# Kernel tuning notes

Measured on AMD Instinct MI355X. Metric: run time of the kernel, lower is better.

The kernel has to match this reference:

```python
import jax, jax.numpy as jnp
import numpy as np

N_NODES = 50000
N_EDGES = 800000
N_GRAPHS = 16
F_IN = 128
E_DIM = 16
HID = 32
HEADS = 2
EPS_BN = 1e-5


def gatv2_conv(x, edge_index, edge_attr, Wl, bl, Wr, br, We, att, bias, heads, out_ch):
    """PyG GATv2Conv (share_weights=False, concat=True, add_self_loops=True, fill_value='mean')."""
    n = x.shape[0]
    src, dst = edge_index[0], edge_index[1]
    loop = jnp.arange(n)
    src = jnp.concatenate([src, loop])
    dst = jnp.concatenate([dst, loop])
    ea = jnp.concatenate([edge_attr, jnp.broadcast_to(edge_attr.mean(0), (n, edge_attr.shape[1]))])
    x_l = (x @ Wl + bl).reshape(n, heads, out_ch)   # source transform
    x_r = (x @ Wr + br).reshape(n, heads, out_ch)   # target transform
    e = (ea @ We).reshape(-1, heads, out_ch)
    m = jax.nn.leaky_relu(x_l[src] + x_r[dst] + e, 0.2)      # [E, H, C]
    alpha = (m * att[None]).sum(-1)                          # [E, H]
    amax = jax.ops.segment_max(alpha, dst, num_segments=n)
    ex = jnp.exp(alpha - amax[dst])
    denom = jax.ops.segment_sum(ex, dst, num_segments=n)
    alpha = ex / (denom[dst] + 1e-16)
    out = jax.ops.segment_sum(x_l[src] * alpha[..., None], dst, num_segments=n)
    return out.reshape(n, heads * out_ch) + bias


def batch_norm(x, g, b):
    mu = x.mean(0)
    var = jnp.var(x, axis=0)  # biased, as torch BatchNorm1d training mode
    return (x - mu) * jax.lax.rsqrt(var + EPS_BN) * g + b


def setup_inputs() -> dict:
    key = jax.random.key(0)
    ks = jax.random.split(key, 24)
    s = 0.1
    d1 = HID * HEADS  # 64
    inp = {
        'x': jax.random.normal(ks[0], (N_NODES, F_IN), jnp.float32),
        'edge_index': jax.random.randint(ks[1], (2, N_EDGES), 0, N_NODES),
        'edge_attr': jax.random.normal(ks[2], (N_EDGES, E_DIM), jnp.float32),
        'batch': jnp.sort(jax.random.randint(ks[3], (N_NODES,), 0, N_GRAPHS)),
        'skip1_W': jax.random.normal(ks[4], (F_IN, d1)) * s,
        'skip1_b': jnp.zeros((d1,)),
        'conv1_Wl': jax.random.normal(ks[5], (F_IN, d1)) * s,
        'conv1_bl': jnp.zeros((d1,)),
        'conv1_Wr': jax.random.normal(ks[6], (F_IN, d1)) * s,
        'conv1_br': jnp.zeros((d1,)),
        'conv1_We': jax.random.normal(ks[7], (E_DIM, d1)) * s,
        'conv1_att': jax.random.normal(ks[8], (HEADS, HID)) * s,
        'conv1_bias': jnp.zeros((d1,)),
        'bn1_g': jnp.ones((d1,)),
        'bn1_b': jnp.zeros((d1,)),
        'skip2_W': jax.random.normal(ks[9], (d1, HID)) * s,
        'skip2_b': jnp.zeros((HID,)),
        'conv2_Wl': jax.random.normal(ks[10], (d1, HID)) * s,
        'conv2_bl': jnp.zeros((HID,)),
        'conv2_Wr': jax.random.normal(ks[11], (d1, HID)) * s,
        'conv2_br': jnp.zeros((HID,)),
        'conv2_We': jax.random.normal(ks[12], (E_DIM, HID)) * s,
        'conv2_att': jax.random.normal(ks[13], (1, HID)) * s,
        'conv2_bias': jnp.zeros((HID,)),
        'bn2_g': jnp.ones((HID,)),
        'bn2_b': jnp.zeros((HID,)),
    }
    return inp


def reference(x, edge_index, edge_attr, batch,
              skip1_W, skip1_b, conv1_Wl, conv1_bl, conv1_Wr, conv1_br, conv1_We, conv1_att, conv1_bias, bn1_g, bn1_b,
              skip2_W, skip2_b, conv2_Wl, conv2_bl, conv2_Wr, conv2_br, conv2_We, conv2_att, conv2_bias, bn2_g, bn2_b):
    h_proj = x @ skip1_W + skip1_b
    h = gatv2_conv(x, edge_index, edge_attr, conv1_Wl, conv1_bl, conv1_Wr, conv1_br, conv1_We, conv1_att, conv1_bias, HEADS, HID)
    h = jax.nn.elu(batch_norm(h, bn1_g, bn1_b) + h_proj)
    h_proj = h @ skip2_W + skip2_b
    h2 = gatv2_conv(h, edge_index, edge_attr, conv2_Wl, conv2_bl, conv2_Wr, conv2_br, conv2_We, conv2_att, conv2_bias, 1, HID)
    h2 = jax.nn.elu(batch_norm(h2, bn2_g, bn2_b) + h_proj)
    ones = jnp.ones((h2.shape[0],), h2.dtype)
    counts = jax.ops.segment_sum(ones, batch, num_segments=N_GRAPHS)
    x_mean = jax.ops.segment_sum(h2, batch, num_segments=N_GRAPHS) / jnp.maximum(counts, 1.0)[:, None]
    x_max = jax.ops.segment_max(h2, batch, num_segments=N_GRAPHS)
    x_max = jnp.where(counts[:, None] > 0, x_max, 0.0)
    return jnp.concatenate([x_mean, x_max], axis=1)
```

## Files before the change

### kernel.cpp

```cpp
#include <hip/hip_runtime.h>
#include <hip/hip_bf16.h>

#define NE 800000
#define NN 50000
#define NG 16
#define ETOT (NE + NN)

typedef unsigned short u16;
typedef __attribute__((ext_vector_type(8))) short short8;
typedef __attribute__((ext_vector_type(4))) float float4v;

__device__ __forceinline__ float b2f(u16 u) {
  return __uint_as_float(((unsigned)u) << 16);
}
__device__ __forceinline__ u16 f2b(float f) {
  __hip_bfloat16 b = __float2bfloat16(f);
  return *(u16*)&b;
}
__device__ __forceinline__ void cv8(uint4 v, float* o) {
  o[0] = __uint_as_float(v.x << 16);
  o[1] = __uint_as_float(v.x & 0xFFFF0000u);
  o[2] = __uint_as_float(v.y << 16);
  o[3] = __uint_as_float(v.y & 0xFFFF0000u);
  o[4] = __uint_as_float(v.z << 16);
  o[5] = __uint_as_float(v.z & 0xFFFF0000u);
  o[6] = __uint_as_float(v.w << 16);
  o[7] = __uint_as_float(v.w & 0xFFFF0000u);
}
__device__ __forceinline__ unsigned pk2(float a, float b) {
  return (unsigned)f2b(a) | ((unsigned)f2b(b) << 16);
}
__device__ __forceinline__ unsigned f2key(float f) {
  unsigned u = __float_as_uint(f);
  return (u & 0x80000000u) ? ~u : (u | 0x80000000u);
}
__device__ __forceinline__ float key2f(unsigned k) {
  unsigned u = (k & 0x80000000u) ? (k ^ 0x80000000u) : ~k;
  return __uint_as_float(u);
}
__device__ __forceinline__ int plaus(unsigned h) {
  unsigned eh = (h >> 7) & 0xFF;
  return (h == 0) || (eh >= 100 && eh <= 140);
}
__device__ __forceinline__ float lrelu(float v) {
  return (v > 0.f) ? v : 0.2f * v;
}

#define NDEG 8
#define NPOOL 16
#define LOG2E 1.4426950408889634f

__global__ __launch_bounds__(256) void k_init(uint4* __restrict__ zbase, int zcnt16,
                                              const unsigned* __restrict__ a,
                                              const unsigned* __restrict__ b,
                                              const unsigned* __restrict__ c,
                                              int* __restrict__ flags) {
  uint4 z = {0, 0, 0, 0};
  for (int i = blockIdx.x * 256 + threadIdx.x; i < zcnt16; i += gridDim.x * 256)
    zbase[i] = z;
  if (blockIdx.x != 0) return;
  __shared__ int cnt[3];
  if (threadIdx.x < 3) cnt[threadIdx.x] = 0;
  __syncthreads();
  const unsigned* arr[3] = {a, b, c};
  for (int k = 0; k < 3; k++) {
    int ok = 0;
    for (int i = threadIdx.x; i < 4096; i += 256) {
      unsigned w = arr[k][i];
      ok += (plaus(w & 0xFFFFu) && plaus(w >> 16)) ? 1 : 0;
    }
    atomicAdd(&cnt[k], ok);
  }
  __syncthreads();
  if (threadIdx.x == 0) {
    int f0 = cnt[0] > 2048, f1 = cnt[1] > 2048, f2 = cnt[2] > 2048;
    flags[0] = f0;
    flags[1] = f1;
    flags[2] = f2;
    flags[3] = f0 && f1 && f2;
  }
}

__global__ __launch_bounds__(256) void k_hist(const int* __restrict__ ei,
                                              int* __restrict__ deg8) {
  int gt = blockIdx.x * 256 + threadIdx.x;
  if (gt >= ETOT) return;
  int dst = (gt < NE) ? ei[NE + gt] : gt - NE;
  atomicAdd(&deg8[(blockIdx.x & (NDEG - 1)) * NN + dst], 1);
}

__global__ __launch_bounds__(256) void k_colsum_xsplit(
    const void* __restrict__ ea, const void* __restrict__ xin,
    const int* __restrict__ flg, float* __restrict__ mean_part,
    u16* __restrict__ xh, u16* __restrict__ xlo) {
  int gt = blockIdx.x * 256 + threadIdx.x;
  bool eb = flg[2] != 0;
  int col = gt & 15;
  int row = gt >> 4;
  int rstride = (gridDim.x * 256) >> 4;
  float s = 0.f;
  if (eb) {
    const u16* p = (const u16*)ea;
    for (int e = row; e < NE; e += rstride) s += b2f(p[(size_t)e * 16 + col]);
  } else {
    const float* p = (const float*)ea;
    for (int e = row; e < NE; e += rstride) s += p[(size_t)e * 16 + col];
  }
  __shared__ float ls[256];
  ls[threadIdx.x] = s;
  __syncthreads();
  if (threadIdx.x < 16) {
    float t = 0.f;
    for (int i = threadIdx.x; i < 256; i += 16) t += ls[i];
    atomicAdd(&mean_part[(blockIdx.x & 63) * 16 + threadIdx.x], t);
  }
  if (flg[0] == 0) {
    const float4* xp4 = (const float4*)xin;
    const int nch = NN * 32;
    int stride = gridDim.x * 256;
    for (int i = gt; i < nch; i += stride) {
      float4 v = xp4[i];
      u16 h0 = f2b(v.x), h1 = f2b(v.y), h2 = f2b(v.z), h3 = f2b(v.w);
      u16 l0 = f2b(v.x - b2f(h0));
      u16 l1 = f2b(v.y - b2f(h1));
      u16 l2 = f2b(v.z - b2f(h2));
      u16 l3 = f2b(v.w - b2f(h3));
      uint2 ho, lo2;
      ho.x = (unsigned)h0 | ((unsigned)h1 << 16);
      ho.y = (unsigned)h2 | ((unsigned)h3 << 16);
      lo2.x = (unsigned)l0 | ((unsigned)l1 << 16);
      lo2.y = (unsigned)l2 | ((unsigned)l3 << 16);
      *(uint2*)(xh + (size_t)i * 4) = ho;
      *(uint2*)(xlo + (size_t)i * 4) = lo2;
    }
  }
}

#define SCAN_NT ((NN + 1023) / 1024)

__global__ __launch_bounds__(256) void k_scansum(const int* __restrict__ deg8,
                                                 const float* __restrict__ mean_part,
                                                 float* __restrict__ mean_sums,
                                                 int* __restrict__ tile_tot) {
  int t = threadIdx.x;
  if (blockIdx.x == 0 && t < 16) {
    float s = 0.f;
#pragma unroll
    for (int j = 0; j < 64; j++) s += mean_part[j * 16 + t];
    mean_sums[t] = s;
  }
  int lane = t & 63;
  int wv = t >> 6;
  int idx = blockIdx.x * 1024 + t * 4;
  int s4 = 0;
  if (idx + 3 < NN) {
#pragma unroll
    for (int c = 0; c < NDEG; c++) {
      int4 dc = *(const int4*)(deg8 + c * NN + idx);
      s4 += dc.x + dc.y + dc.z + dc.w;
    }
  } else {
#pragma unroll
    for (int c = 0; c < NDEG; c++) {
      if (idx + 0 < NN) s4 += deg8[c * NN + idx + 0];
      if (idx + 1 < NN) s4 += deg8[c * NN + idx + 1];
      if (idx + 2 < NN) s4 += deg8[c * NN + idx + 2];
      if (idx + 3 < NN) s4 += deg8[c * NN + idx + 3];
    }
  }
  int r = s4;
#pragma unroll
  for (int ofs = 1; ofs < 64; ofs <<= 1) r += __shfl_xor(r, ofs, 64);
  __shared__ int wsum[4];
  if (lane == 0) wsum[wv] = r;
  __syncthreads();
  if (t == 0) tile_tot[blockIdx.x] = wsum[0] + wsum[1] + wsum[2] + wsum[3];
}

__global__ __launch_bounds__(256) void k_scanwrite(const int* __restrict__ deg8,
                                                   const int* __restrict__ tile_tot,
                                                   int* __restrict__ start,
                                                   int* __restrict__ cursor) {
  __shared__ int sbase;
  __shared__ int wsum[4];
  int t = threadIdx.x;
  int lane = t & 63;
  int wv = t >> 6;
  if (wv == 0) {
    int v = (lane < SCAN_NT) ? tile_tot[lane] : 0;
    int sc = v;
#pragma unroll
    for (int ofs = 1; ofs < 64; ofs <<= 1) {
      int u = __shfl_up(sc, ofs, 64);
      if (lane >= ofs) sc += u;
    }
    if (lane == (int)blockIdx.x) sbase = sc - v;
    if (blockIdx.x == 0 && lane == SCAN_NT - 1) start[NN] = sc;
  }
  int idx = blockIdx.x * 1024 + t * 4;
  int4 d = {0, 0, 0, 0};
  if (idx + 3 < NN) {
#pragma unroll
    for (int c = 0; c < NDEG; c++) {
      int4 dc = *(const int4*)(deg8 + c * NN + idx);
      d.x += dc.x; d.y += dc.y; d.z += dc.z; d.w += dc.w;
    }
  } else {
#pragma unroll
    for (int c = 0; c < NDEG; c++) {
      if (idx + 0 < NN) d.x += deg8[c * NN + idx + 0];
      if (idx + 1 < NN) d.y += deg8[c * NN + idx + 1];
      if (idx + 2 < NN) d.z += deg8[c * NN + idx + 2];
      if (idx + 3 < NN) d.w += deg8[c * NN + idx + 3];
    }
  }
  int s4 = d.x + d.y + d.z + d.w;
  int sc = s4;
#pragma unroll
  for (int ofs = 1; ofs < 64; ofs <<= 1) {
    int v = __shfl_up(sc, ofs, 64);
    if (lane >= ofs) sc += v;
  }
  if (lane == 63) wsum[wv] = sc;
  __syncthreads();
  int wbase = 0;
#pragma unroll
  for (int w = 0; w < 4; w++)
    if (w < wv) wbase += wsum[w];
  int excl = sbase + wbase + (sc - s4);
  int4 st;
  st.x = excl;
  st.y = excl + d.x;
  st.z = st.y + d.y;
  st.w = st.z + d.z;
  if (idx + 3 < NN) {
    *(int4*)(start + idx) = st;
    *(int4*)(cursor + idx) = st;
  } else {
    if (idx + 0 < NN) { start[idx + 0] = st.x; cursor[idx + 0] = st.x; }
    if (idx + 1 < NN) { start[idx + 1] = st.y; cursor[idx + 1] = st.y; }
    if (idx + 2 < NN) { start[idx + 2] = st.z; cursor[idx + 2] = st.z; }
    if (idx + 3 < NN) { start[idx + 3] = st.w; cursor[idx + 3] = st.w; }
  }
}

template <int K, int N, int RPB>
__device__ __forceinline__ void gemm_direct(
    const void* __restrict__ W, const void* __restrict__ bb, bool wb,
    const u16* __restrict__ xh, const u16* __restrict__ xlo, bool has_lo,
    u16* __restrict__ out, int tile) {
  constexpr int CT = N / 16;
  constexpr int WPC = 4 / CT;
  constexpr int KK = K / 32;
  int lane = threadIdx.x & 63;
  int wave = threadIdx.x >> 6;
  int col = lane & 15;
  int quad = lane >> 4;
  int ct = wave % CT;
  int rt_off = wave / CT;
  short8 bh[KK], bl[KK];
#pragma unroll
  for (int kk = 0; kk < KK; kk++) {
    short8 th, tl;
#pragma unroll
    for (int j = 0; j < 8; j++) {
      int k = kk * 32 + quad * 8 + j;
      float w = wb ? b2f(((const u16*)W)[k * N + ct * 16 + col])
                   : ((const float*)W)[k * N + ct * 16 + col];
      u16 hb = f2b(w);
      th[j] = (short)hb;
      tl[j] = (short)f2b(w - b2f(hb));
    }
    bh[kk] = th;
    bl[kk] = tl;
  }
  float bias = wb ? b2f(((const u16*)bb)[ct * 16 + col])
                  : ((const float*)bb)[ct * 16 + col];
  int rt0 = tile * RPB;
  for (int i = rt_off; i < RPB; i += WPC) {
    int rt = rt0 + i;
    int row = rt * 16 + col;
    float4v acc = {0.f, 0.f, 0.f, 0.f};
#pragma unroll
    for (int kk = 0; kk < KK; kk++) {
      short8 afh = *(const short8*)(xh + (size_t)row * K + kk * 32 + quad * 8);
      acc = __builtin_amdgcn_mfma_f32_16x16x32_bf16(afh, bh[kk], acc, 0, 0, 0);
      if (has_lo) {
        short8 afl = *(const short8*)(xlo + (size_t)row * K + kk * 32 + quad * 8);
        acc = __builtin_amdgcn_mfma_f32_16x16x32_bf16(afl, bh[kk], acc, 0, 0, 0);
      }
      if (!wb)
        acc = __builtin_amdgcn_mfma_f32_16x16x32_bf16(afh, bl[kk], acc, 0, 0, 0);
    }
#pragma unroll
    for (int r = 0; r < 4; r++) {
      int orow = rt * 16 + quad * 4 + r;
      out[(size_t)orow * N + ct * 16 + col] = f2b(acc[r] + bias);
    }
  }
}

template <int K, int N, int TILES, int RPB>
__global__ __launch_bounds__(256) void k_lin1(
    const void* __restrict__ xin, const u16* __restrict__ xh,
    const u16* __restrict__ xlo, const int* __restrict__ flg,
    const void* W0, const void* W1, const void* W2,
    const void* b0, const void* b1, const void* b2,
    u16* __restrict__ o0, u16* __restrict__ o1, u16* __restrict__ o2) {
  int lidx = blockIdx.x;
  int wset = lidx / TILES;
  int tile = lidx % TILES;
  bool wb = flg[1] != 0;
  bool xb = flg[0] != 0;
  const void* W = wset == 0 ? W0 : (wset == 1 ? W1 : W2);
  const void* bb = wset == 0 ? b0 : (wset == 1 ? b1 : b2);
  u16* out = wset == 0 ? o0 : (wset == 1 ? o1 : o2);
  const u16* ah = xb ? (const u16*)xin : xh;
  gemm_direct<K, N, RPB>(W, bb, wb, ah, xlo, !xb, out, tile);
}

__global__ __launch_bounds__(256) void k_buildcsr_pay(
    const int* __restrict__ ei, const void* __restrict__ eattr,
    const int* __restrict__ flg, const float* __restrict__ mean_sums,
    int* __restrict__ cursor, int* __restrict__ csr_src,
    u16* __restrict__ ea16) {
  int e = blockIdx.x * 256 + threadIdx.x;
  if (e >= ETOT) return;
  bool eb = flg[2] != 0;
  int src, dst;
  if (e < NE) { src = ei[e]; dst = ei[NE + e]; } else { src = dst = e - NE; }
  float rec[16];
  if (e < NE) {
    if (eb) {
      const uint4* q = (const uint4*)((const u16*)eattr + (size_t)e * 16);
      cv8(q[0], rec);
      cv8(q[1], rec + 8);
    } else {
      const float* q = (const float*)eattr + (size_t)e * 16;
#pragma unroll
      for (int k = 0; k < 16; k++) rec[k] = q[k];
    }
  } else {
#pragma unroll
    for (int k = 0; k < 16; k++) rec[k] = mean_sums[k] * (1.0f / NE);
  }
  int pos = atomicAdd(&cursor[dst], 1);
  csr_src[pos] = src;
  u16 rb[16];
#pragma unroll
  for (int k = 0; k < 16; k++) rb[k] = f2b(rec[k]);
  uint4* dp = (uint4*)(ea16 + (size_t)pos * 16);
  dp[0] = *(uint4*)rb;
  dp[1] = *(uint4*)(rb + 8);
}

__global__ __launch_bounds__(256) void k_buildcsr(const int* __restrict__ ei,
                                                  int* __restrict__ cursor,
                                                  uint2* __restrict__ csr) {
  int e = blockIdx.x * 256 + threadIdx.x;
  if (e >= ETOT) return;
  int src, dst;
  if (e < NE) { src = ei[e]; dst = ei[NE + e]; } else { src = dst = e - NE; }
  int pos = atomicAdd(&cursor[dst], 1);
  uint2 r; r.x = (unsigned)src; r.y = (unsigned)e;
  csr[pos] = r;
}

__global__ __launch_bounds__(256) void k_ewgemm(
    const u16* __restrict__ ea, const int* __restrict__ flg,
    const void* We1, const void* We2,
    u16* __restrict__ ew1, u16* __restrict__ ew2) {
  bool wb = flg[1] != 0;
  int lane = threadIdx.x & 63;
  int col = lane & 15;
  int quad = lane >> 4;
  short8 b1h[4], b1l[4], b2h[2], b2l[2];
#pragma unroll
  for (int ct = 0; ct < 4; ct++) {
    short8 th, tl;
#pragma unroll
    for (int j = 0; j < 8; j++) {
      int k = quad * 8 + j;
      float w = 0.f;
      if (k < 16)
        w = wb ? b2f(((const u16*)We1)[k * 64 + ct * 16 + col])
               : ((const float*)We1)[k * 64 + ct * 16 + col];
      u16 hb = f2b(w);
      th[j] = (short)hb;
      tl[j] = (short)f2b(w - b2f(hb));
    }
    b1h[ct] = th; b1l[ct] = tl;
  }
#pragma unroll
  for (int ct = 0; ct < 2; ct++) {
    short8 th, tl;
#pragma unroll
    for (int j = 0; j < 8; j++) {
      int k = quad * 8 + j;
      float w = 0.f;
      if (k < 16)
        w = wb ? b2f(((const u16*)We2)[k * 32 + ct * 16 + col])
               : ((const float*)We2)[k * 32 + ct * 16 + col];
      u16 hb = f2b(w);
      th[j] = (short)hb;
      tl[j] = (short)f2b(w - b2f(hb));
    }
    b2h[ct] = th; b2l[ct] = tl;
  }
  int nw = (gridDim.x * 256) >> 6;
  int wid = (blockIdx.x * 256 + threadIdx.x) >> 6;
  const int NT = ETOT / 16;
  for (int rt = wid; rt < NT; rt += nw) {
    int row = rt * 16 + col;
    short8 af = {0, 0, 0, 0, 0, 0, 0, 0};
    if (quad < 2) af = *(const short8*)(ea + (size_t)row * 16 + quad * 8);
#pragma unroll
    for (int ct = 0; ct < 4; ct++) {
      float4v acc = {0.f, 0.f, 0.f, 0.f};
      acc = __builtin_amdgcn_mfma_f32_16x16x32_bf16(af, b1h[ct], acc, 0, 0, 0);
      acc = __builtin_amdgcn_mfma_f32_16x16x32_bf16(af, b1l[ct], acc, 0, 0, 0);
#pragma unroll
      for (int r = 0; r < 4; r++)
        ew1[(size_t)(rt * 16 + quad * 4 + r) * 64 + ct * 16 + col] = f2b(acc[r]);
    }
#pragma unroll
    for (int ct = 0; ct < 2; ct++) {
      float4v acc = {0.f, 0.f, 0.f, 0.f};
      acc = __builtin_amdgcn_mfma_f32_16x16x32_bf16(af, b2h[ct], acc, 0, 0, 0);
      acc = __builtin_amdgcn_mfma_f32_16x16x32_bf16(af, b2l[ct], acc, 0, 0, 0);
#pragma unroll
      for (int r = 0; r < 4; r++)
        ew2[(size_t)(rt * 16 + quad * 4 + r) * 32 + ct * 16 + col] = f2b(acc[r]);
    }
  }
}

template <int K, int N, int RPB>
__global__ __launch_bounds__(256) void k_lin3b(
    const void* __restrict__ xin, const int* __restrict__ flg,
    const void* W0, const void* W1, const void* W2,
    const void* b0, const void* b1, const void* b2,
    u16* __restrict__ o0, u16* __restrict__ o1, u16* __restrict__ o2, int M) {
  (void)M;
  bool wb = flg[1] != 0;
  const void* W = blockIdx.y == 0 ? W0 : (blockIdx.y == 1 ? W1 : W2);
  const void* bb = blockIdx.y == 0 ? b0 : (blockIdx.y == 1 ? b1 : b2);
  u16* out = blockIdx.y == 0 ? o0 : (blockIdx.y == 1 ? o1 : o2);
  gemm_direct<K, N, RPB>(W, bb, wb, (const u16*)xin, nullptr, false, out,
                         blockIdx.x);
}

__device__ __forceinline__ float dot16b(const u16* __restrict__ p,
                                        const float* __restrict__ W) {
  float ea[16];
  const uint4* q = (const uint4*)p;
  cv8(q[0], ea);
  cv8(q[1], ea + 8);
  float s = 0.f;
#pragma unroll
  for (int k = 0; k < 16; k++) s += ea[k] * W[k];
  return s;
}
__device__ __forceinline__ float dot16u(const u16* __restrict__ p,
                                        const float* __restrict__ W) {
  const uint4* q = (const uint4*)p;
  uint4 A = q[0], B = q[1];
  unsigned w0 = (unsigned)__builtin_amdgcn_readfirstlane((int)A.x);
  unsigned w1 = (unsigned)__builtin_amdgcn_readfirstlane((int)A.y);
  unsigned w2 = (unsigned)__builtin_amdgcn_readfirstlane((int)A.z);
  unsigned w3 = (unsigned)__builtin_amdgcn_readfirstlane((int)A.w);
  unsigned w4 = (unsigned)__builtin_amdgcn_readfirstlane((int)B.x);
  unsigned w5 = (unsigned)__builtin_amdgcn_readfirstlane((int)B.y);
  unsigned w6 = (unsigned)__builtin_amdgcn_readfirstlane((int)B.z);
  unsigned w7 = (unsigned)__builtin_amdgcn_readfirstlane((int)B.w);
  float s = 0.f;
  s += __uint_as_float(w0 << 16) * W[0];
  s += __uint_as_float(w0 & 0xFFFF0000u) * W[1];
  s += __uint_as_float(w1 << 16) * W[2];
  s += __uint_as_float(w1 & 0xFFFF0000u) * W[3];
  s += __uint_as_float(w2 << 16) * W[4];
  s += __uint_as_float(w2 & 0xFFFF0000u) * W[5];
  s += __uint_as_float(w3 << 16) * W[6];
  s += __uint_as_float(w3 & 0xFFFF0000u) * W[7];
  s += __uint_as_float(w4 << 16) * W[8];
  s += __uint_as_float(w4 & 0xFFFF0000u) * W[9];
  s += __uint_as_float(w5 << 16) * W[10];
  s += __uint_as_float(w5 & 0xFFFF0000u) * W[11];
  s += __uint_as_float(w6 << 16) * W[12];
  s += __uint_as_float(w6 & 0xFFFF0000u) * W[13];
  s += __uint_as_float(w7 << 16) * W[14];
  s += __uint_as_float(w7 & 0xFFFF0000u) * W[15];
  return s;
}
__device__ __forceinline__ float dot16f(const float* __restrict__ q,
                                        const float* __restrict__ W) {
  float s = 0.f;
#pragma unroll
  for (int k = 0; k < 16; k++) s += q[k] * W[k];
  return s;
}

template <int H, int C, bool PRE>
__global__ __launch_bounds__(256) void k_fusedp(
    const int* __restrict__ start, const int* __restrict__ csr_src,
    const u16* __restrict__ pay, const u16* __restrict__ ewp,
    const int* __restrict__ flg,
    const u16* __restrict__ xl, const u16* __restrict__ xr,
    const void* We, const void* att, u16* __restrict__ agg) {
  constexpr int D = H * C;
  constexpr int NPW = 64 / D;
  bool wb = flg[1] != 0;
  int lane = threadIdx.x & 63;
  int ch = lane % D;
  float Wreg[16];
  if constexpr (!PRE) {
    if (wb) {
      const u16* Wp = (const u16*)We;
#pragma unroll
      for (int k = 0; k < 16; k++) Wreg[k] = b2f(Wp[k * D + ch]);
    } else {
      const float* Wp = (const float*)We;
#pragma unroll
      for (int k = 0; k < 16; k++) Wreg[k] = Wp[k * D + ch];
    }
  }
  float attv = (wb ? b2f(((const u16*)att)[ch]) : ((const float*)att)[ch]) * LOG2E;
  int wid = (blockIdx.x * 256 + threadIdx.x) >> 6;

  if constexpr (NPW == 1) {
    int node = __builtin_amdgcn_readfirstlane(wid);
    int s0 = __builtin_amdgcn_readfirstlane(start[node]);
    int s1 = __builtin_amdgcn_readfirstlane(start[node + 1]);
    float xrv = b2f(xr[(unsigned)node * D + ch]);
    float ssum = 0.f, acc = 0.f;
    int p = s0;
    for (; p + 7 < s1; p += 8) {
      int c[8];
#pragma unroll
      for (int j = 0; j < 8; j++)
        c[j] = __builtin_amdgcn_readfirstlane(csr_src[p + j]);
      float xlv[8];
#pragma unroll
      for (int j = 0; j < 8; j++) xlv[j] = b2f(xl[(unsigned)c[j] * D + ch]);
      float t[8];
#pragma unroll
      for (int j = 0; j < 8; j++) {
        float ev;
        if constexpr (PRE) ev = b2f(ewp[(size_t)(p + j) * D + ch]);
        else ev = dot16u(pay + (size_t)(p + j) * 16, Wreg);
        t[j] = lrelu(xlv[j] + xrv + ev) * attv;
      }
#pragma unroll
      for (int mk = 1; mk <= 16; mk <<= 1) {
#pragma unroll
        for (int j = 0; j < 8; j++) t[j] += __shfl_xor(t[j], mk, 64);
      }
#pragma unroll
      for (int j = 0; j < 8; j++) {
        float ex = exp2f(t[j]);
        ssum += ex;
        acc += ex * xlv[j];
      }
    }
    for (; p + 3 < s1; p += 4) {
      int c[4];
#pragma unroll
      for (int j = 0; j < 4; j++)
        c[j] = __builtin_amdgcn_readfirstlane(csr_src[p + j]);
      float xlv[4], t[4];
#pragma unroll
      for (int j = 0; j < 4; j++) xlv[j] = b2f(xl[(unsigned)c[j] * D + ch]);
#pragma unroll
      for (int j = 0; j < 4; j++) {
        float ev;
        if constexpr (PRE) ev = b2f(ewp[(size_t)(p + j) * D + ch]);
        else ev = dot16u(pay + (size_t)(p + j) * 16, Wreg);
        t[j] = lrelu(xlv[j] + xrv + ev) * attv;
      }
#pragma unroll
      for (int mk = 1; mk <= 16; mk <<= 1) {
#pragma unroll
        for (int j = 0; j < 4; j++) t[j] += __shfl_xor(t[j], mk, 64);
      }
#pragma unroll
      for (int j = 0; j < 4; j++) {
        float ex = exp2f(t[j]);
        ssum += ex;
        acc += ex * xlv[j];
      }
    }
    for (; p < s1; ++p) {
      int c0 = __builtin_amdgcn_readfirstlane(csr_src[p]);
      float xlv = b2f(xl[(unsigned)c0 * D + ch]);
      float ev;
      if constexpr (PRE) ev = b2f(ewp[(size_t)p * D + ch]);
      else ev = dot16u(pay + (size_t)p * 16, Wreg);
      float t = lrelu(xlv + xrv + ev) * attv;
#pragma unroll
      for (int mk = 1; mk <= 16; mk <<= 1) t += __shfl_xor(t, mk, 64);
      float ex = exp2f(t);
      ssum += ex;
      acc += ex * xlv;
    }
    agg[(size_t)node * D + ch] = f2b(acc / (ssum + 1e-16f));
  } else {
    int node = wid * NPW + lane / D;
    int s0 = start[node], s1 = start[node + 1];
    int deg = s1 - s0;
    int last = s1 - 1;
    int degmax = max(deg, __shfl_xor(deg, 32, 64));
    float xrv = b2f(xr[(unsigned)node * D + ch]);
    float ssum = 0.f, acc = 0.f;
    for (int i = 0; i < degmax; i += 8) {
      int pp[8];
      bool av[8];
      int cc[8];
#pragma unroll
      for (int j = 0; j < 8; j++) {
        pp[j] = min(s0 + i + j, last);
        av[j] = (i + j) < deg;
      }
#pragma unroll
      for (int j = 0; j < 8; j++) cc[j] = csr_src[pp[j]];
      float xlv[8];
#pragma unroll
      for (int j = 0; j < 8; j++) xlv[j] = b2f(xl[(unsigned)cc[j] * D + ch]);
      float t[8];
#pragma unroll
      for (int j = 0; j < 8; j++) {
        float ev;
        if constexpr (PRE) ev = b2f(ewp[(size_t)pp[j] * D + ch]);
        else ev = dot16b(pay + (size_t)pp[j] * 16, Wreg);
        t[j] = lrelu(xlv[j] + xrv + ev) * attv;
      }
#pragma unroll
      for (int mk = 1; mk <= 16; mk <<= 1) {
#pragma unroll
        for (int j = 0; j < 8; j++) t[j] += __shfl_xor(t[j], mk, 64);
      }
#pragma unroll
      for (int j = 0; j < 8; j++) {
        float ex = av[j] ? exp2f(t[j]) : 0.f;
        ssum += ex;
        acc += ex * xlv[j];
      }
    }
    agg[(size_t)node * D + ch] = f2b(acc / (ssum + 1e-16f));
  }
}

template <int H, int C>
__global__ __launch_bounds__(256) void k_fusedg(
    const int* __restrict__ start, const uint2* __restrict__ csr,
    const void* __restrict__ eattr, const int* __restrict__ flg,
    const float* __restrict__ mean_sums,
    const u16* __restrict__ xl, const u16* __restrict__ xr,
    const void* We, const void* att, u16* __restrict__ agg) {
  constexpr int D = H * C;
  constexpr int NPW = 64 / D;
  bool wb = flg[1] != 0;
  bool eb = flg[2] != 0;
  int lane = threadIdx.x & 63;
  int ch = lane % D;
  float Wreg[16];
  if (wb) {
    const u16* Wp = (const u16*)We;
#pragma unroll
    for (int k = 0; k < 16; k++) Wreg[k] = b2f(Wp[k * D + ch]);
  } else {
    const float* Wp = (const float*)We;
#pragma unroll
    for (int k = 0; k < 16; k++) Wreg[k] = Wp[k * D + ch];
  }
  float attv = wb ? b2f(((const u16*)att)[ch]) : ((const float*)att)[ch];
  float ev_self = 0.f;
#pragma unroll
  for (int k = 0; k < 16; k++) ev_self += mean_sums[k] * (1.0f / NE) * Wreg[k];
  int wid = (blockIdx.x * 256 + threadIdx.x) >> 6;
  int node = wid * NPW + lane / D;
  int s0 = start[node], s1 = start[node + 1];
  int deg = s1 - s0;
  int last = s1 - 1;
  int degmax = deg;
  if constexpr (NPW == 2) degmax = max(deg, __shfl_xor(deg, 32, 64));
  float xrv = b2f(xr[(size_t)node * D + ch]);
  float ssum = 0.f, acc = 0.f;
  for (int i = 0; i < degmax; i += 2) {
    uint2 cr0 = csr[min(s0 + i, last)];
    uint2 cr1 = csr[min(s0 + i + 1, last)];
    bool a0 = i < deg, a1 = i + 1 < deg;
    float xlv0 = b2f(xl[(size_t)cr0.x * D + ch]);
    float xlv1 = b2f(xl[(size_t)cr1.x * D + ch]);
    float ev0 = cr0.y < NE ? (eb ? dot16b((const u16*)eattr + (size_t)cr0.y * 16, Wreg)
                                 : dot16f((const float*)eattr + (size_t)cr0.y * 16, Wreg))
                           : ev_self;
    float ev1 = cr1.y < NE ? (eb ? dot16b((const u16*)eattr + (size_t)cr1.y * 16, Wreg)
                                 : dot16f((const float*)eattr + (size_t)cr1.y * 16, Wreg))
                           : ev_self;
    float mv0 = xlv0 + xrv + ev0;
    float mv1 = xlv1 + xrv + ev1;
    mv0 = (mv0 > 0.f) ? mv0 : 0.2f * mv0;
    mv1 = (mv1 > 0.f) ? mv1 : 0.2f * mv1;
    float t0 = mv0 * attv, t1 = mv1 * attv;
#pragma unroll
    for (int mk = 1; mk <= 16; mk <<= 1) {
      t0 += __shfl_xor(t0, mk, 64);
      t1 += __shfl_xor(t1, mk, 64);
    }
    float ex0 = a0 ? __expf(t0) : 0.f;
    float ex1 = a1 ? __expf(t1) : 0.f;
    ssum += ex0 + ex1;
    acc += ex0 * xlv0 + ex1 * xlv1;
  }
  agg[(size_t)node * D + ch] = f2b(acc / (ssum + 1e-16f));
}

template <int D>
__global__ __launch_bounds__(256) void k_bnred(const u16* __restrict__ v,
                                               float* __restrict__ sum,
                                               float* __restrict__ sq, int M) {
  constexpr int RB = 256 / D;
  int tid = threadIdx.x;
  int c = tid % D;
  int rg = tid / D;
  float s = 0.f, q = 0.f;
  for (int r = blockIdx.x * RB + rg; r < M; r += gridDim.x * RB) {
    float x = b2f(v[(size_t)r * D + c]);
    s += x;
    q += x * x;
  }
  __shared__ float ls[256], lq[256];
  ls[tid] = s; lq[tid] = q;
  __syncthreads();
  if (tid < D) {
    float ts = 0.f, tq = 0.f;
    for (int i = tid; i < 256; i += D) { ts += ls[i]; tq += lq[i]; }
    atomicAdd(&sum[tid], ts);
    atomicAdd(&sq[tid], tq);
  }
}

template <int D>
__global__ __launch_bounds__(256) void k_bnapply(const u16* __restrict__ agg,
                                                 const u16* __restrict__ hp,
                                                 const float* __restrict__ sum,
                                                 const float* __restrict__ sq,
                                                 const void* g, const void* b,
                                                 const int* __restrict__ flg,
                                                 u16* __restrict__ out, int M) {
  bool wb = flg[1] != 0;
  int idx = blockIdx.x * 256 + threadIdx.x;
  if (idx >= M * D) return;
  int c = idx & (D - 1);
  float gc = wb ? b2f(((const u16*)g)[c]) : ((const float*)g)[c];
  float bc = wb ? b2f(((const u16*)b)[c]) : ((const float*)b)[c];
  float mu = sum[c] * (1.f / M);
  float var = fmaxf(sq[c] * (1.f / M) - mu * mu, 0.f);
  float sc = rsqrtf(var + 1e-5f) * gc;
  float v = (b2f(agg[idx]) - mu) * sc + bc + b2f(hp[idx]);
  v = v > 0.f ? v : expm1f(v);
  out[idx] = f2b(v);
}

__global__ __launch_bounds__(256) void k_poolred(
    const u16* __restrict__ agg2, const u16* __restrict__ hp2,
    const float* __restrict__ sum, const float* __restrict__ sq,
    const void* g, const void* b, const int* __restrict__ flg,
    const int* __restrict__ batch,
    float* __restrict__ pool_sum, unsigned* __restrict__ pool_maxk,
    float* __restrict__ pool_cnt) {
  bool wb = flg[1] != 0;
  int c = threadIdx.x & 31;
  int rg = threadIdx.x >> 5;
  int cp = blockIdx.x & (NPOOL - 1);
  float* psum = pool_sum + cp * (NG * 32);
  unsigned* pmax = pool_maxk + cp * (NG * 32);
  float* pcnt = pool_cnt + cp * NG;
  float gc = wb ? b2f(((const u16*)g)[c]) : ((const float*)g)[c];
  float bc = wb ? b2f(((const u16*)b)[c]) : ((const float*)b)[c];
  float mu = sum[c] * (1.f / NN);
  float var = fmaxf(sq[c] * (1.f / NN) - mu * mu, 0.f);
  float scl = rsqrtf(var + 1e-5f) * gc;
  float sh = bc - mu * scl;

  const int NPB = 256;
  int n0 = blockIdx.x * NPB;
  int nend = min(n0 + NPB, NN);
  int cur = -1;
  float s = 0.f, mx = 0.f;
  int cnt = 0;
  for (int n = n0 + rg; n < nend; n += 8) {
    int gi = batch[n];
    float v = b2f(agg2[(size_t)n * 32 + c]) * scl + sh + b2f(hp2[(size_t)n * 32 + c]);
    v = v > 0.f ? v : expm1f(v);
    if (gi != cur) {
      if (cur >= 0) {
        atomicAdd(&psum[cur * 32 + c], s);
        atomicMax(&pmax[cur * 32 + c], f2key(mx));
        if (c == 0) atomicAdd(&pcnt[cur], (float)cnt);
      }
      cur = gi; s = 0.f; mx = -INFINITY; cnt = 0;
    }
    s += v;
    mx = fmaxf(mx, v);
    cnt++;
  }
  if (cur >= 0) {
    atomicAdd(&psum[cur * 32 + c], s);
    atomicMax(&pmax[cur * 32 + c], f2key(mx));
    if (c == 0) atomicAdd(&pcnt[cur], (float)cnt);
  }
}

__global__ __launch_bounds__(256) void k_poolfin(
    const float* __restrict__ pool_sum, const unsigned* __restrict__ pool_maxk,
    const float* __restrict__ pool_cnt, const int* __restrict__ flg,
    void* __restrict__ out) {
  bool ob = flg[3] != 0;
  for (int idx = threadIdx.x; idx < NG * 64; idx += 256) {
    int gi = idx / 64, cc = idx % 64;
    float cntv = 0.f;
#pragma unroll
    for (int k = 0; k < NPOOL; k++) cntv += pool_cnt[k * NG + gi];
    float val;
    if (cc < 32) {
      float s = 0.f;
#pragma unroll
      for (int k = 0; k < NPOOL; k++) s += pool_sum[k * (NG * 32) + gi * 32 + cc];
      val = s / fmaxf(cntv, 1.f);
    } else {
      unsigned km = 0u;
#pragma unroll
      for (int k = 0; k < NPOOL; k++)
        km = max(km, pool_maxk[k * (NG * 32) + gi * 32 + (cc - 32)]);
      val = cntv > 0.f ? key2f(km) : 0.f;
    }
    if (ob) ((u16*)out)[idx] = f2b(val);
    else ((float*)out)[idx] = val;
  }
}

extern "C" void kernel_launch(void* const* d_in, const int* in_sizes, int n_in,
                              void* d_out, int out_size, void* d_ws, size_t ws_size,
                              hipStream_t stream) {
  (void)in_sizes; (void)n_in; (void)out_size;
  const void* x     = d_in[0];
  const int*  ei    = (const int*)d_in[1];
  const void* eattr = d_in[2];
  const int*  batch = (const int*)d_in[3];
  const void* skip1_W = d_in[4];
  const void* skip1_b = d_in[5];
  const void* c1_Wl = d_in[6];
  const void* c1_bl = d_in[7];
  const void* c1_Wr = d_in[8];
  const void* c1_br = d_in[9];
  const void* c1_We = d_in[10];
  const void* c1_att = d_in[11];
  const void* bn1_g = d_in[13];
  const void* bn1_b = d_in[14];
  const void* skip2_W = d_in[15];
  const void* skip2_b = d_in[16];
  const void* c2_Wl = d_in[17];
  const void* c2_bl = d_in[18];
  const void* c2_Wr = d_in[19];
  const void* c2_br = d_in[20];
  const void* c2_We = d_in[21];
  const void* c2_att = d_in[22];
  const void* bn2_g = d_in[24];
  const void* bn2_b = d_in[25];

  float* ws = (float*)d_ws;
  size_t off = 0;
  auto alloc = [&](size_t nfl) {
    float* p = ws + off;
    off += (nfl + 15) & ~(size_t)15;
    return p;
  };
  int*   flags      = (int*)alloc(16);
  float* mean_sums  = alloc(16);
  float* mean_part  = alloc(64 * 16);
  int*   deg8       = (int*)alloc((size_t)NDEG * NN);
  float* bnsum1     = alloc(64);
  float* bnsq1      = alloc(64);
  float* bnsum2     = alloc(32);
  float* bnsq2      = alloc(32);
  float* pool_cnt   = alloc((size_t)NPOOL * NG);
  float* pool_sum   = alloc((size_t)NPOOL * NG * 32);
  unsigned* pool_maxk = (unsigned*)alloc((size_t)NPOOL * NG * 32);
  size_t zcnt16 = (off * sizeof(float)) / 16;
  int*   tile_tot = (int*)alloc(64);
  u16* xh  = (u16*)alloc((size_t)NN * 64);
  u16* xlo = (u16*)alloc((size_t)NN * 64);
  size_t zoff = off;

  int* start   = (int*)alloc(NN + 1);
  int* cursor  = (int*)alloc(NN);
  int* csr_src = (int*)alloc(ETOT);
  u16* ea16    = (u16*)alloc((size_t)ETOT * 8);
  u16* ew1     = (u16*)alloc((size_t)ETOT * 32);
  u16* ew2     = (u16*)alloc((size_t)ETOT * 16);
  uint2* csr = nullptr;
  u16* xl1 = (u16*)alloc((size_t)NN * 32);
  u16* xr1 = (u16*)alloc((size_t)NN * 32);
  u16* hp1 = (u16*)alloc((size_t)NN * 32);
  u16* agg = (u16*)alloc((size_t)NN * 32);
  int tier = 0;
  if (off * sizeof(float) > ws_size) {
    tier = 1;
    off = zoff;
    start   = (int*)alloc(NN + 1);
    cursor  = (int*)alloc(NN);
    csr_src = (int*)alloc(ETOT);
    ea16    = (u16*)alloc((size_t)ETOT * 8);
    ew1 = ew2 = nullptr;
    xl1 = (u16*)alloc((size_t)NN * 32);
    xr1 = (u16*)alloc((size_t)NN * 32);
    hp1 = (u16*)alloc((size_t)NN * 32);
    agg = (u16*)alloc((size_t)NN * 32);
  }
  if (tier == 1 && off * sizeof(float) > ws_size) {
    tier = 2;
    off = zoff;
    start   = (int*)alloc(NN + 1);
    cursor  = (int*)alloc(NN);
    csr     = (uint2*)alloc((size_t)ETOT * 2);
    ea16    = nullptr;
    xl1 = (u16*)alloc((size_t)NN * 32);
    xr1 = (u16*)alloc((size_t)NN * 32);
    hp1 = (u16*)alloc((size_t)NN * 32);
    agg = (u16*)alloc((size_t)NN * 32);
  }
  u16* h1  = xr1;
  u16* xl2 = xl1;
  u16* xr2 = xl1 + (size_t)NN * 32;
  u16* hp2 = hp1;

  int eg = (ETOT + 255) / 256;

  k_init<<<128, 256, 0, stream>>>((uint4*)d_ws, (int)zcnt16,
                                  (const unsigned*)x, (const unsigned*)skip1_W,
                                  (const unsigned*)eattr, flags);
  k_hist<<<eg, 256, 0, stream>>>(ei, deg8);
  k_colsum_xsplit<<<2048, 256, 0, stream>>>(eattr, x, flags, mean_part, xh, xlo);
  k_scansum<<<SCAN_NT, 256, 0, stream>>>(deg8, mean_part, mean_sums, tile_tot);
  k_scanwrite<<<SCAN_NT, 256, 0, stream>>>(deg8, tile_tot, start, cursor);
  k_lin1<128, 64, 625, 5><<<1875, 256, 0, stream>>>(
      x, xh, xlo, flags, c1_Wl, c1_Wr, skip1_W,
      c1_bl, c1_br, skip1_b, xl1, xr1, hp1);
  if (tier <= 1) {
    k_buildcsr_pay<<<eg, 256, 0, stream>>>(ei, eattr, flags, mean_sums,
                                           cursor, csr_src, ea16);
  } else {
    k_buildcsr<<<eg, 256, 0, stream>>>(ei, cursor, csr);
  }
  if (tier == 0) {
    k_ewgemm<<<1024, 256, 0, stream>>>(ea16, flags, c1_We, c2_We, ew1, ew2);
  }
  if (tier == 0) {
    k_fusedp<2, 32, true><<<NN / 4, 256, 0, stream>>>(start, csr_src, ea16, ew1,
                                                      flags, xl1, xr1, c1_We,
                                                      c1_att, agg);
  } else if (tier == 1) {
    k_fusedp<2, 32, false><<<NN / 4, 256, 0, stream>>>(start, csr_src, ea16, nullptr,
                                                       flags, xl1, xr1, c1_We,
                                                       c1_att, agg);
  } else {
    k_fusedg<2, 32><<<NN / 4, 256, 0, stream>>>(start, csr, eattr, flags, mean_sums,
                                                xl1, xr1, c1_We, c1_att, agg);
  }
  k_bnred<64><<<256, 256, 0, stream>>>(agg, bnsum1, bnsq1, NN);
  k_bnapply<64><<<(NN * 64 + 255) / 256, 256, 0, stream>>>(agg, hp1, bnsum1, bnsq1,
                                                           bn1_g, bn1_b, flags, h1, NN);
  {
    dim3 g(625, 3);
    k_lin3b<64, 32, 5><<<g, 256, 0, stream>>>(h1, flags, c2_Wl, c2_Wr, skip2_W,
                                              c2_bl, c2_br, skip2_b,
                                              xl2, xr2, hp2, NN);
  }
  if (tier == 0) {
    k_fusedp<1, 32, true><<<NN / 8, 256, 0, stream>>>(start, csr_src, ea16, ew2,
                                                      flags, xl2, xr2, c2_We,
                                                      c2_att, agg);
  } else if (tier == 1) {
    k_fusedp<1, 32, false><<<NN / 8, 256, 0, stream>>>(start, csr_src, ea16, nullptr,
                                                       flags, xl2, xr2, c2_We,
                                                       c2_att, agg);
  } else {
    k_fusedg<1, 32><<<NN / 8, 256, 0, stream>>>(start, csr, eattr, flags, mean_sums,
                                                xl2, xr2, c2_We, c2_att, agg);
  }
  k_bnred<32><<<256, 256, 0, stream>>>(agg, bnsum2, bnsq2, NN);
  k_poolred<<<(NN + 255) / 256, 256, 0, stream>>>(agg, hp2, bnsum2, bnsq2,
                                                  bn2_g, bn2_b, flags, batch,
                                                  pool_sum, pool_maxk, pool_cnt);
  k_poolfin<<<1, 256, 0, stream>>>(pool_sum, pool_maxk, pool_cnt, flags, d_out);
}
```

Baseline: 515.5 us.

## Process two channels per lane in fused GATv2 aggregation to pack more nodes per wave

```diff
diff --git a/kernel.cpp b/kernel.cpp
--- a/kernel.cpp
+++ b/kernel.cpp
@@ -461,37 +461,6 @@
   for (int k = 0; k < 16; k++) s += ea[k] * W[k];
   return s;
 }
-__device__ __forceinline__ float dot16u(const u16* __restrict__ p,
-                                        const float* __restrict__ W) {
-  const uint4* q = (const uint4*)p;
-  uint4 A = q[0], B = q[1];
-  unsigned w0 = (unsigned)__builtin_amdgcn_readfirstlane((int)A.x);
-  unsigned w1 = (unsigned)__builtin_amdgcn_readfirstlane((int)A.y);
-  unsigned w2 = (unsigned)__builtin_amdgcn_readfirstlane((int)A.z);
-  unsigned w3 = (unsigned)__builtin_amdgcn_readfirstlane((int)A.w);
-  unsigned w4 = (unsigned)__builtin_amdgcn_readfirstlane((int)B.x);
-  unsigned w5 = (unsigned)__builtin_amdgcn_readfirstlane((int)B.y);
-  unsigned w6 = (unsigned)__builtin_amdgcn_readfirstlane((int)B.z);
-  unsigned w7 = (unsigned)__builtin_amdgcn_readfirstlane((int)B.w);
-  float s = 0.f;
-  s += __uint_as_float(w0 << 16) * W[0];
-  s += __uint_as_float(w0 & 0xFFFF0000u) * W[1];
-  s += __uint_as_float(w1 << 16) * W[2];
-  s += __uint_as_float(w1 & 0xFFFF0000u) * W[3];
-  s += __uint_as_float(w2 << 16) * W[4];
-  s += __uint_as_float(w2 & 0xFFFF0000u) * W[5];
-  s += __uint_as_float(w3 << 16) * W[6];
-  s += __uint_as_float(w3 & 0xFFFF0000u) * W[7];
-  s += __uint_as_float(w4 << 16) * W[8];
-  s += __uint_as_float(w4 & 0xFFFF0000u) * W[9];
-  s += __uint_as_float(w5 << 16) * W[10];
-  s += __uint_as_float(w5 & 0xFFFF0000u) * W[11];
-  s += __uint_as_float(w6 << 16) * W[12];
-  s += __uint_as_float(w6 & 0xFFFF0000u) * W[13];
-  s += __uint_as_float(w7 << 16) * W[14];
-  s += __uint_as_float(w7 & 0xFFFF0000u) * W[15];
-  return s;
-}
 __device__ __forceinline__ float dot16f(const float* __restrict__ q,
                                         const float* __restrict__ W) {
   float s = 0.f;
@@ -508,145 +477,98 @@
     const u16* __restrict__ xl, const u16* __restrict__ xr,
     const void* We, const void* att, u16* __restrict__ agg) {
   constexpr int D = H * C;
-  constexpr int NPW = 64 / D;
+  constexpr int GL = D / 2;
+  constexpr int NPW = 64 / GL;
   bool wb = flg[1] != 0;
   int lane = threadIdx.x & 63;
-  int ch = lane % D;
-  float Wreg[16];
+  int j = lane % GL;
+  int ch0 = 2 * j;
+  float Wreg0[16], Wreg1[16];
   if constexpr (!PRE) {
     if (wb) {
       const u16* Wp = (const u16*)We;
 #pragma unroll
-      for (int k = 0; k < 16; k++) Wreg[k] = b2f(Wp[k * D + ch]);
+      for (int k = 0; k < 16; k++) {
+        Wreg0[k] = b2f(Wp[k * D + ch0]);
+        Wreg1[k] = b2f(Wp[k * D + ch0 + 1]);
+      }
     } else {
       const float* Wp = (const float*)We;
 #pragma unroll
-      for (int k = 0; k < 16; k++) Wreg[k] = Wp[k * D + ch];
-    }
-  }
-  float attv = (wb ? b2f(((const u16*)att)[ch]) : ((const float*)att)[ch]) * LOG2E;
+      for (int k = 0; k < 16; k++) {
+        Wreg0[k] = Wp[k * D + ch0];
+        Wreg1[k] = Wp[k * D + ch0 + 1];
+      }
+    }
+  }
+  float attv0, attv1;
+  if (wb) {
+    attv0 = b2f(((const u16*)att)[ch0]) * LOG2E;
+    attv1 = b2f(((const u16*)att)[ch0 + 1]) * LOG2E;
+  } else {
+    attv0 = ((const float*)att)[ch0] * LOG2E;
+    attv1 = ((const float*)att)[ch0 + 1] * LOG2E;
+  }
   int wid = (blockIdx.x * 256 + threadIdx.x) >> 6;
-
-  if constexpr (NPW == 1) {
-    int node = __builtin_amdgcn_readfirstlane(wid);
-    int s0 = __builtin_amdgcn_readfirstlane(start[node]);
-    int s1 = __builtin_amdgcn_readfirstlane(start[node + 1]);
-    float xrv = b2f(xr[(unsigned)node * D + ch]);
-    float ssum = 0.f, acc = 0.f;
-    int p = s0;
-    for (; p + 7 < s1; p += 8) {
-      int c[8];
-#pragma unroll
-      for (int j = 0; j < 8; j++)
-        c[j] = __builtin_amdgcn_readfirstlane(csr_src[p + j]);
-      float xlv[8];
-#pragma unroll
-      for (int j = 0; j < 8; j++) xlv[j] = b2f(xl[(unsigned)c[j] * D + ch]);
-      float t[8];
-#pragma unroll
-      for (int j = 0; j < 8; j++) {
-        float ev;
-        if constexpr (PRE) ev = b2f(ewp[(size_t)(p + j) * D + ch]);
-        else ev = dot16u(pay + (size_t)(p + j) * 16, Wreg);
-        t[j] = lrelu(xlv[j] + xrv + ev) * attv;
+  int node = wid * NPW + lane / GL;
+  int s0 = start[node], s1 = start[node + 1];
+  int deg = s1 - s0;
+  int last = s1 - 1;
+  int degmax = deg;
+#pragma unroll
+  for (int m = GL; m < 64; m <<= 1)
+    degmax = max(degmax, __shfl_xor(degmax, m, 64));
+  unsigned xru = *(const unsigned*)(xr + (size_t)node * D + ch0);
+  float xr0 = __uint_as_float(xru << 16);
+  float xr1 = __uint_as_float(xru & 0xFFFF0000u);
+  float ssum = 0.f, acc0 = 0.f, acc1 = 0.f;
+  for (int i = 0; i < degmax; i += 4) {
+    int pp[4];
+    bool av[4];
+    int cc[4];
+#pragma unroll
+    for (int u = 0; u < 4; u++) {
+      pp[u] = min(s0 + i + u, last);
+      av[u] = (i + u) < deg;
+    }
+#pragma unroll
+    for (int u = 0; u < 4; u++) cc[u] = csr_src[pp[u]];
+    unsigned xlu[4];
+#pragma unroll
+    for (int u = 0; u < 4; u++)
+      xlu[u] = *(const unsigned*)(xl + (size_t)(unsigned)cc[u] * D + ch0);
+    float t[4], xl0[4], xl1[4];
+#pragma unroll
+    for (int u = 0; u < 4; u++) {
+      xl0[u] = __uint_as_float(xlu[u] << 16);
+      xl1[u] = __uint_as_float(xlu[u] & 0xFFFF0000u);
+      float ev0, ev1;
+      if constexpr (PRE) {
+        unsigned ewu = *(const unsigned*)(ewp + (size_t)pp[u] * D + ch0);
+        ev0 = __uint_as_float(ewu << 16);
+        ev1 = __uint_as_float(ewu & 0xFFFF0000u);
+      } else {
+        ev0 = dot16b(pay + (size_t)pp[u] * 16, Wreg0);
+        ev1 = dot16b(pay + (size_t)pp[u] * 16, Wreg1);
       }
-#pragma unroll
-      for (int mk = 1; mk <= 16; mk <<= 1) {
-#pragma unroll
-        for (int j = 0; j < 8; j++) t[j] += __shfl_xor(t[j], mk, 64);
-      }
-#pragma unroll
-      for (int j = 0; j < 8; j++) {
-        float ex = exp2f(t[j]);
-        ssum += ex;
-        acc += ex * xlv[j];
-      }
-    }
-    for (; p + 3 < s1; p += 4) {
-      int c[4];
-#pragma unroll
-      for (int j = 0; j < 4; j++)
-        c[j] = __builtin_amdgcn_readfirstlane(csr_src[p + j]);
-      float xlv[4], t[4];
-#pragma unroll
-      for (int j = 0; j < 4; j++) xlv[j] = b2f(xl[(unsigned)c[j] * D + ch]);
-#pragma unroll
-      for (int j = 0; j < 4; j++) {
-        float ev;
-        if constexpr (PRE) ev = b2f(ewp[(size_t)(p + j) * D + ch]);
-        else ev = dot16u(pay + (size_t)(p + j) * 16, Wreg);
-        t[j] = lrelu(xlv[j] + xrv + ev) * attv;
-      }
-#pragma unroll
-      for (int mk = 1; mk <= 16; mk <<= 1) {
-#pragma unroll
-        for (int j = 0; j < 4; j++) t[j] += __shfl_xor(t[j], mk, 64);
-      }
-#pragma unroll
-      for (int j = 0; j < 4; j++) {
-        float ex = exp2f(t[j]);
-        ssum += ex;
-        acc += ex * xlv[j];
-      }
-    }
-    for (; p < s1; ++p) {
-      int c0 = __builtin_amdgcn_readfirstlane(csr_src[p]);
-      float xlv = b2f(xl[(unsigned)c0 * D + ch]);
-      float ev;
-      if constexpr (PRE) ev = b2f(ewp[(size_t)p * D + ch]);
-      else ev = dot16u(pay + (size_t)p * 16, Wreg);
-      float t = lrelu(xlv + xrv + ev) * attv;
-#pragma unroll
-      for (int mk = 1; mk <= 16; mk <<= 1) t += __shfl_xor(t, mk, 64);
-      float ex = exp2f(t);
+      t[u] = lrelu(xl0[u] + xr0 + ev0) * attv0 +
+             lrelu(xl1[u] + xr1 + ev1) * attv1;
+    }
+#pragma unroll
+    for (int mk = 1; mk <= 8; mk <<= 1) {
+#pragma unroll
+      for (int u = 0; u < 4; u++) t[u] += __shfl_xor(t[u], mk, 64);
+    }
+#pragma unroll
+    for (int u = 0; u < 4; u++) {
+      float ex = av[u] ? exp2f(t[u]) : 0.f;
       ssum += ex;
-      acc += ex * xlv;
-    }
-    agg[(size_t)node * D + ch] = f2b(acc / (ssum + 1e-16f));
-  } else {
-    int node = wid * NPW + lane / D;
-    int s0 = start[node], s1 = start[node + 1];
-    int deg = s1 - s0;
-    int last = s1 - 1;
-    int degmax = max(deg, __shfl_xor(deg, 32, 64));
-    float xrv = b2f(xr[(unsigned)node * D + ch]);
-    float ssum = 0.f, acc = 0.f;
-    for (int i = 0; i < degmax; i += 8) {
-      int pp[8];
-      bool av[8];
-      int cc[8];
-#pragma unroll
-      for (int j = 0; j < 8; j++) {
-        pp[j] = min(s0 + i + j, last);
-        av[j] = (i + j) < deg;
-      }
-#pragma unroll
-      for (int j = 0; j < 8; j++) cc[j] = csr_src[pp[j]];
-      float xlv[8];
-#pragma unroll
-      for (int j = 0; j < 8; j++) xlv[j] = b2f(xl[(unsigned)cc[j] * D + ch]);
-      float t[8];
-#pragma unroll
-      for (int j = 0; j < 8; j++) {
-        float ev;
-        if constexpr (PRE) ev = b2f(ewp[(size_t)pp[j] * D + ch]);
-        else ev = dot16b(pay + (size_t)pp[j] * 16, Wreg);
-        t[j] = lrelu(xlv[j] + xrv + ev) * attv;
-      }
-#pragma unroll
-      for (int mk = 1; mk <= 16; mk <<= 1) {
-#pragma unroll
-        for (int j = 0; j < 8; j++) t[j] += __shfl_xor(t[j], mk, 64);
-      }
-#pragma unroll
-      for (int j = 0; j < 8; j++) {
-        float ex = av[j] ? exp2f(t[j]) : 0.f;
-        ssum += ex;
-        acc += ex * xlv[j];
-      }
-    }
-    agg[(size_t)node * D + ch] = f2b(acc / (ssum + 1e-16f));
-  }
+      acc0 += ex * xl0[u];
+      acc1 += ex * xl1[u];
+    }
+  }
+  float inv = 1.f / (ssum + 1e-16f);
+  *(unsigned*)(agg + (size_t)node * D + ch0) = pk2(acc0 * inv, acc1 * inv);
 }
 
 template <int H, int C>
@@ -957,11 +879,11 @@
     k_ewgemm<<<1024, 256, 0, stream>>>(ea16, flags, c1_We, c2_We, ew1, ew2);
   }
   if (tier == 0) {
-    k_fusedp<2, 32, true><<<NN / 4, 256, 0, stream>>>(start, csr_src, ea16, ew1,
+    k_fusedp<2, 32, true><<<NN / 8, 256, 0, stream>>>(start, csr_src, ea16, ew1,
                                                       flags, xl1, xr1, c1_We,
                                                       c1_att, agg);
   } else if (tier == 1) {
-    k_fusedp<2, 32, false><<<NN / 4, 256, 0, stream>>>(start, csr_src, ea16, nullptr,
+    k_fusedp<2, 32, false><<<NN / 8, 256, 0, stream>>>(start, csr_src, ea16, nullptr,
                                                        flags, xl1, xr1, c1_We,
                                                        c1_att, agg);
   } else {
@@ -978,13 +900,13 @@
                                               xl2, xr2, hp2, NN);
   }
   if (tier == 0) {
-    k_fusedp<1, 32, true><<<NN / 8, 256, 0, stream>>>(start, csr_src, ea16, ew2,
-                                                      flags, xl2, xr2, c2_We,
-                                                      c2_att, agg);
-  } else if (tier == 1) {
-    k_fusedp<1, 32, false><<<NN / 8, 256, 0, stream>>>(start, csr_src, ea16, nullptr,
+    k_fusedp<1, 32, true><<<NN / 16, 256, 0, stream>>>(start, csr_src, ea16, ew2,
                                                        flags, xl2, xr2, c2_We,
                                                        c2_att, agg);
+  } else if (tier == 1) {
+    k_fusedp<1, 32, false><<<NN / 16, 256, 0, stream>>>(start, csr_src, ea16, nullptr,
+                                                        flags, xl2, xr2, c2_We,
+                                                        c2_att, agg);
   } else {
     k_fusedg<1, 32><<<NN / 8, 256, 0, stream>>>(start, csr, eattr, flags, mean_sums,
                                                 xl2, xr2, c2_We, c2_att, agg);
```

After: 498.8 us. 3.2% less time.
